# Kernel optimization log

Measured on AMD Instinct MI355X. Metric: run time of the kernel, lower is better.

## Reference

```python
import jax, jax.numpy as jnp
import numpy as np

N = 131072      # 8192 sudoku puzzles x 16 cells
E = 1048576     # random constraint edges (avg degree 8)
HID = 64
NEG_SLOPE = 0.2


def setup_inputs() -> dict:
    key = jax.random.key(0)
    ks = jax.random.split(key, 18)
    p = lambda k, shape: jax.random.normal(k, shape, dtype=jnp.float32) * 0.05
    return {
        "x": jax.random.randint(ks[0], (N,), 0, 5),
        "edge_index": jax.random.randint(ks[1], (2, E), 0, N),
        "emb": p(ks[2], (5, HID)),
        # conv1: in 64 -> heads=4, C=64, concat
        "W1": p(ks[3], (HID, 4 * HID)),
        "a1_src": p(ks[4], (4, HID)),
        "a1_dst": p(ks[5], (4, HID)),
        "b1": p(ks[6], (4 * HID,)),
        # conv2: in 256 -> heads=4, C=64, concat
        "W2": p(ks[7], (4 * HID, 4 * HID)),
        "a2_src": p(ks[8], (4, HID)),
        "a2_dst": p(ks[9], (4, HID)),
        "b2": p(ks[10], (4 * HID,)),
        # conv3: in 256 -> heads=1, C=64, no concat
        "W3": p(ks[11], (4 * HID, HID)),
        "a3_src": p(ks[12], (1, HID)),
        "a3_dst": p(ks[13], (1, HID)),
        "b3": p(ks[14], (HID,)),
        "fc_w": p(ks[15], (HID, 5)),
        "fc_b": p(ks[16], (5,)),
    }


def gat_conv(x, src, dst, W, a_src, a_dst, b, concat):
    """PyG-style GATConv (self-loops already appended to src/dst)."""
    n = x.shape[0]
    H, C = a_src.shape
    h = (x @ W).reshape(n, H, C)                       # [N,H,C]
    alpha_s = jnp.einsum('nhc,hc->nh', h, a_src)       # [N,H]
    alpha_d = jnp.einsum('nhc,hc->nh', h, a_dst)
    e = jax.nn.leaky_relu(alpha_s[src] + alpha_d[dst], NEG_SLOPE)  # [E,H]
    # scatter-softmax over incoming edges per destination node
    e_max = jax.ops.segment_max(e, dst, num_segments=n)
    e_exp = jnp.exp(e - e_max[dst])
    denom = jax.ops.segment_sum(e_exp, dst, num_segments=n)
    alpha = e_exp / (denom[dst] + 1e-16)               # [E,H]
    msg = h[src] * alpha[:, :, None]                   # [E,H,C]
    out = jax.ops.segment_sum(msg, dst, num_segments=n)  # [N,H,C]
    out = out.reshape(n, H * C) if concat else out.mean(axis=1)
    return out + b


def reference(x, edge_index, emb, W1, a1_src, a1_dst, b1,
              W2, a2_src, a2_dst, b2, W3, a3_src, a3_dst, b3, fc_w, fc_b):
    n = x.shape[0]
    loops = jnp.arange(n)
    src = jnp.concatenate([edge_index[0], loops])  # add self-loops (PyG default)
    dst = jnp.concatenate([edge_index[1], loops])
    h = emb[x]                                                    # [N,64]
    h = jax.nn.elu(gat_conv(h, src, dst, W1, a1_src, a1_dst, b1, True))
    h = jax.nn.elu(gat_conv(h, src, dst, W2, a2_src, a2_dst, b2, True))
    h = jax.nn.elu(gat_conv(h, src, dst, W3, a3_src, a3_dst, b3, False))
    return h @ fc_w + fc_b                                        # [N,5]
```

## Files before the change

### kernel.cpp

```cpp
#include <hip/hip_runtime.h>
#include <hip/hip_bf16.h>
#include <hip/hip_fp8.h>

typedef __attribute__((ext_vector_type(8))) short short8;
typedef __attribute__((ext_vector_type(4))) short short4_t;
typedef __attribute__((ext_vector_type(4))) float floatx4;
typedef __attribute__((ext_vector_type(2))) float floatx2;

constexpr int NB  = 256;
constexpr int CAP = 6144;

__device__ __forceinline__ unsigned short f2bf(float f){
  unsigned int u = __float_as_uint(f);
  u += 0x7FFF + ((u >> 16) & 1);
  return (unsigned short)(u >> 16);
}
__device__ __forceinline__ float bf2f(unsigned short h){
  return __uint_as_float(((unsigned int)h) << 16);
}
__device__ __forceinline__ float lrelu(float x){ return x > 0.f ? x : 0.2f * x; }
__device__ __forceinline__ float eluf(float x){ return x > 0.f ? x : (__expf(x) - 1.f); }

__device__ __forceinline__ unsigned char f2fp8(float f){
  __hip_fp8_e4m3 t(f);
  return (unsigned char)t.__x;
}
__device__ __forceinline__ float fp82f(unsigned char b){
  __hip_fp8_e4m3 t;
  t.__x = (__hip_fp8_storage_t)b;
  return (float)t;
}

template<bool HI>
__device__ __forceinline__ floatx2 fp8pk2(unsigned int v){
#if defined(__has_builtin) && __has_builtin(__builtin_amdgcn_cvt_pk_f32_fp8)
  return __builtin_amdgcn_cvt_pk_f32_fp8((int)v, HI);
#else
  floatx2 r;
  constexpr int sh = HI ? 16 : 0;
  r.x = fp82f((unsigned char)((v >> sh) & 0xFF));
  r.y = fp82f((unsigned char)((v >> (sh + 8)) & 0xFF));
  return r;
#endif
}

__device__ __forceinline__ unsigned int f32x4_to_fp8(float a0, float a1, float a2, float a3){
#if defined(__has_builtin) && __has_builtin(__builtin_amdgcn_cvt_pk_fp8_f32)
  int w = 0;
  w = __builtin_amdgcn_cvt_pk_fp8_f32(a0, a1, w, false);
  w = __builtin_amdgcn_cvt_pk_fp8_f32(a2, a3, w, true);
  return (unsigned int)w;
#else
  return (unsigned int)f2fp8(a0) | ((unsigned int)f2fp8(a1) << 8) |
         ((unsigned int)f2fp8(a2) << 16) | ((unsigned int)f2fp8(a3) << 24);
#endif
}

__device__ __forceinline__ void gload16(const unsigned short* g, unsigned short* l){
  __builtin_amdgcn_global_load_lds(
      (const __attribute__((address_space(1))) unsigned int*)(const void*)g,
      (__attribute__((address_space(3))) unsigned int*)(void*)l,
      16, 0, 0);
}


__global__ __launch_bounds__(256) void part_k(const int* __restrict__ ei, int E, int shift,
                                              int* __restrict__ gcnt,
                                              uint2* __restrict__ bbuf){
  __shared__ int hist[NB];
  __shared__ int base[NB];
  int tid = threadIdx.x;
  hist[tid] = 0;
  __syncthreads();
  int blk_start = blockIdx.x * 4096;
  int src[16], bkt[16], lp[16];
  #pragma unroll
  for (int k = 0; k < 16; k++){
    int i = blk_start + k * 256 + tid;
    if (i < E){
      int dst = ei[E + i];
      src[k] = ei[i];
      bkt[k] = dst >> shift;
      lp[k] = atomicAdd(&hist[bkt[k]], 1);
    } else {
      bkt[k] = -1;
    }
  }
  __syncthreads();
  base[tid] = atomicAdd(&gcnt[tid], hist[tid]);
  __syncthreads();
  #pragma unroll
  for (int k = 0; k < 16; k++){
    int i = blk_start + k * 256 + tid;
    if (i < E){
      int b = bkt[k];
      int dst = ei[E + i];
      bbuf[(size_t)b * CAP + base[b] + lp[k]] = make_uint2((unsigned)src[k], (unsigned)dst);
    }
  }
}

__global__ __launch_bounds__(256) void bscan_k(const int* __restrict__ gcnt,
                                               int* __restrict__ gbase,
                                               int* __restrict__ row_ptr, int N, int dpb){
  __shared__ int s[NB];
  int t = threadIdx.x;
  int v = gcnt[t] + dpb;
  s[t] = v;
  __syncthreads();
  #pragma unroll
  for (int off = 1; off < NB; off <<= 1){
    int u = (t >= off) ? s[t - off] : 0;
    __syncthreads();
    s[t] += u;
    __syncthreads();
  }
  gbase[t] = s[t] - v;
  if (t == NB - 1){ gbase[NB] = s[t]; row_ptr[N] = s[t]; }
}

__global__ __launch_bounds__(256) void sort_k(const uint2* __restrict__ bbuf,
                                              const int* __restrict__ gcnt,
                                              const int* __restrict__ gbase,
                                              int* __restrict__ row_ptr,
                                              int* __restrict__ sorted_src, int dpb){
  __shared__ int counts[512];
  __shared__ int curs[512];
  __shared__ int wsum[256];
  __shared__ int sortedL[CAP + 512];
  int b = blockIdx.x, tid = threadIdx.x;
  int cnt = gcnt[b];
  int dstBase = b * dpb;
  int gb = gbase[b];
  counts[tid] = 0;
  counts[tid + 256] = 0;
  __syncthreads();
  for (int i = tid; i < cnt; i += 256){
    uint2 p = bbuf[(size_t)b * CAP + i];
    atomicAdd(&counts[(int)p.y - dstBase], 1);
  }
  __syncthreads();
  int c0 = counts[2 * tid] + 1;
  int c1 = counts[2 * tid + 1] + 1;
  int sum = c0 + c1;
  wsum[tid] = sum;
  __syncthreads();
  #pragma unroll
  for (int off = 1; off < 256; off <<= 1){
    int u = (tid >= off) ? wsum[tid - off] : 0;
    __syncthreads();
    wsum[tid] += u;
    __syncthreads();
  }
  int ex = wsum[tid] - sum;
  int ro0 = ex, ro1 = ex + c0;
  curs[2 * tid] = ro0 + 1;
  curs[2 * tid + 1] = ro1 + 1;
  sortedL[ro0] = dstBase + 2 * tid;
  sortedL[ro1] = dstBase + 2 * tid + 1;
  row_ptr[dstBase + 2 * tid] = gb + ro0;
  row_ptr[dstBase + 2 * tid + 1] = gb + ro1;
  __syncthreads();
  for (int i = tid; i < cnt; i += 256){
    uint2 p = bbuf[(size_t)b * CAP + i];
    int pos = atomicAdd(&curs[(int)p.y - dstBase], 1);
    sortedL[pos] = (int)p.x;
  }
  __syncthreads();
  int tot = cnt + dpb;
  for (int i = tid; i < tot; i += 256) sorted_src[gb + i] = sortedL[i];
}


__global__ __launch_bounds__(256) void prep_k(const float* __restrict__ W2,
                                              unsigned short* __restrict__ Wp2,
                                              const float* __restrict__ W3,
                                              unsigned short* __restrict__ Wp3,
                                              const float* __restrict__ emb,
                                              const float* __restrict__ W1,
                                              const float* __restrict__ a1s,
                                              const float* __restrict__ a1d,
                                              float* __restrict__ T1,
                                              float* __restrict__ wt_tab){
  __shared__ float t_lds[1280];
  __shared__ float as_l[20], ad_l[20];
  int b = blockIdx.x;
  int tid = threadIdx.x;
  if (b < 256){
    int idx = b * 256 + tid;
    int k = idx >> 8, nn = idx & 255;
    Wp2[nn * 256 + k] = f2bf(W2[idx]);
  } else if (b < 320){
    int idx = (b - 256) * 256 + tid;
    int k = idx >> 6, nn = idx & 63;
    Wp3[nn * 256 + k] = f2bf(W3[idx]);
  } else {
    for (int i = tid; i < 1280; i += 256){
      int r = i >> 8, c = i & 255;
      float s = 0.f;
      for (int k = 0; k < 64; k++) s += emb[r * 64 + k] * W1[k * 256 + c];
      t_lds[i] = s;
      T1[i] = s;
    }
    __syncthreads();
    if (tid < 20){
      int r = tid >> 2, hh = tid & 3;
      float ss = 0.f, sd = 0.f;
      for (int c = 0; c < 64; c++){
        float f = t_lds[r * 256 + hh * 64 + c];
        ss += f * a1s[hh * 64 + c];
        sd += f * a1d[hh * 64 + c];
      }
      as_l[tid] = ss;
      ad_l[tid] = sd;
    }
    __syncthreads();
    if (tid < 100){
      int xd = tid / 20, rest = tid % 20;
      int h = rest & 3;
      wt_tab[tid] = __expf(lrelu(as_l[rest] + ad_l[xd * 4 + h]));
    }
  }
}

template<int BN, int MODE, bool F8OUT>
__global__ __launch_bounds__(256) void gemm_lds_k(const unsigned short* __restrict__ A,
                                                  const unsigned short* __restrict__ Wp,
                                                  void* __restrict__ Cout, int Nc,
                                                  const float* __restrict__ a_src,
                                                  const float* __restrict__ a_dst,
                                                  float* __restrict__ as_arr,
                                                  float* __restrict__ ad_arr){
  constexpr int K = 256;
  constexpr int NT = BN / 32;
  __shared__ unsigned short Alds[128 * 32];
  __shared__ unsigned short Blds[BN * 32];
  __shared__ float asl[128], adl[128];
  __shared__ float pas[128][2], pad[128][2];
  int tid = threadIdx.x;
  int w = tid >> 6, l = tid & 63;
  int r16 = l & 15, quad = l >> 4;
  int wr = w >> 1, wc = w & 1;
  int mBase = blockIdx.x * 128;
  int nBase = blockIdx.y * BN;

  if constexpr (MODE == 1){
    if (tid < 128){ asl[tid] = a_src[nBase + tid]; adl[tid] = a_dst[nBase + tid]; }
  }
  if constexpr (MODE == 2){
    if (tid < 64){ asl[tid] = a_src[tid]; adl[tid] = a_dst[tid]; }
  }

  int arow = l >> 2;
  int kcol = (l & 3) * 8;
  const unsigned short* gA0 = A + (size_t)(mBase + w * 32 + arow) * K + kcol;
  const unsigned short* gA1 = gA0 + (size_t)16 * K;
  unsigned short* lA0 = &Alds[(w * 32) * 32];
  unsigned short* lA1 = &Alds[(w * 32 + 16) * 32];
  const unsigned short* gB0;
  const unsigned short* gB1 = nullptr;
  unsigned short* lB0;
  unsigned short* lB1 = nullptr;
  if constexpr (BN == 128){
    gB0 = Wp + (size_t)(nBase + w * 32 + arow) * K + kcol;
    gB1 = gB0 + (size_t)16 * K;
    lB0 = &Blds[(w * 32) * 32];
    lB1 = &Blds[(w * 32 + 16) * 32];
  } else {
    gB0 = Wp + (size_t)(nBase + w * 16 + arow) * K + kcol;
    lB0 = &Blds[(w * 16) * 32];
  }

  floatx4 acc[4][NT];
  #pragma unroll
  for (int mt = 0; mt < 4; mt++)
    #pragma unroll
    for (int nt = 0; nt < NT; nt++){ floatx4 z = {0.f,0.f,0.f,0.f}; acc[mt][nt] = z; }

  for (int kt = 0; kt < 8; kt++){
    int ko = kt * 32;
    gload16(gA0 + ko, lA0);
    gload16(gA1 + ko, lA1);
    gload16(gB0 + ko, lB0);
    if constexpr (BN == 128) gload16(gB1 + ko, lB1);
    __syncthreads();
    short8 af[4], bfr[NT];
    #pragma unroll
    for (int mt = 0; mt < 4; mt++)
      af[mt] = *(const short8*)&Alds[(wr * 64 + mt * 16 + r16) * 32 + quad * 8];
    #pragma unroll
    for (int nt = 0; nt < NT; nt++)
      bfr[nt] = *(const short8*)&Blds[(wc * (BN / 2) + nt * 16 + r16) * 32 + quad * 8];
    #pragma unroll
    for (int mt = 0; mt < 4; mt++)
      #pragma unroll
      for (int nt = 0; nt < NT; nt++)
        acc[mt][nt] = __builtin_amdgcn_mfma_f32_16x16x32_bf16(af[mt], bfr[nt], acc[mt][nt], 0, 0, 0);
    __syncthreads();
  }

  #pragma unroll
  for (int mt = 0; mt < 4; mt++){
    #pragma unroll
    for (int nt = 0; nt < NT; nt++){
      if constexpr (F8OUT){
        unsigned int pk = f32x4_to_fp8(acc[mt][nt][0] * 64.f, acc[mt][nt][1] * 64.f,
                                       acc[mt][nt][2] * 64.f, acc[mt][nt][3] * 64.f);
        int col = nBase + wc * (BN / 2) + nt * 16 + r16;
        int row0 = mBase + wr * 64 + mt * 16 + quad * 4;
        #pragma unroll
        for (int r = 0; r < 4; r++)
          ((unsigned char*)Cout)[(size_t)(row0 + r) * Nc + col] =
              (unsigned char)((pk >> (r * 8)) & 0xFF);
      } else {
        #pragma unroll
        for (int r = 0; r < 4; r++){
          int row = mBase + wr * 64 + mt * 16 + quad * 4 + r;
          int col = nBase + wc * (BN / 2) + nt * 16 + r16;
          ((unsigned short*)Cout)[(size_t)row * Nc + col] = f2bf(acc[mt][nt][r]);
        }
      }
    }
  }
  if constexpr (MODE == 1){
    int head = (nBase + wc * 64) >> 6;
    #pragma unroll
    for (int mt = 0; mt < 4; mt++){
      #pragma unroll
      for (int r = 0; r < 4; r++){
        float ps = 0.f, pd = 0.f;
        #pragma unroll
        for (int nt = 0; nt < NT; nt++){
          float v = acc[mt][nt][r];
          int ci = wc * 64 + nt * 16 + r16;
          ps += v * asl[ci];
          pd += v * adl[ci];
        }
        ps += __shfl_xor(ps, 1, 64); ps += __shfl_xor(ps, 2, 64);
        ps += __shfl_xor(ps, 4, 64); ps += __shfl_xor(ps, 8, 64);
        pd += __shfl_xor(pd, 1, 64); pd += __shfl_xor(pd, 2, 64);
        pd += __shfl_xor(pd, 4, 64); pd += __shfl_xor(pd, 8, 64);
        if (r16 == 0){
          int row = mBase + wr * 64 + mt * 16 + quad * 4 + r;
          as_arr[row * 4 + head] = ps;
          ad_arr[row * 4 + head] = pd;
        }
      }
    }
  }
  if constexpr (MODE == 2){
    #pragma unroll
    for (int mt = 0; mt < 4; mt++){
      #pragma unroll
      for (int r = 0; r < 4; r++){
        float ps = 0.f, pd = 0.f;
        #pragma unroll
        for (int nt = 0; nt < NT; nt++){
          float v = acc[mt][nt][r];
          int ci = wc * 32 + nt * 16 + r16;
          ps += v * asl[ci];
          pd += v * adl[ci];
        }
        ps += __shfl_xor(ps, 1, 64); ps += __shfl_xor(ps, 2, 64);
        ps += __shfl_xor(ps, 4, 64); ps += __shfl_xor(ps, 8, 64);
        pd += __shfl_xor(pd, 1, 64); pd += __shfl_xor(pd, 2, 64);
        pd += __shfl_xor(pd, 4, 64); pd += __shfl_xor(pd, 8, 64);
        if (r16 == 0){
          int lr = wr * 64 + mt * 16 + quad * 4 + r;
          pas[lr][wc] = ps;
          pad[lr][wc] = pd;
        }
      }
    }
    __syncthreads();
    if (tid < 128){
      as_arr[mBase + tid] = pas[tid][0] + pas[tid][1];
      ad_arr[mBase + tid] = pad[tid][0] + pad[tid][1];
    }
  }
}


__global__ __launch_bounds__(256) void agg1_k(const int* __restrict__ x,
                                              const float* __restrict__ T1,
                                              const float* __restrict__ wt_tab,
                                              const int* __restrict__ row_ptr,
                                              const int* __restrict__ sorted_src,
                                              const float* __restrict__ bias,
                                              unsigned short* __restrict__ outb){
  __shared__ float t_lds[1280];
  __shared__ float wt_l[100], b_lds[256];
  __shared__ float cnt_lds[256][5];
  __shared__ int xd_lds[256];
  int tid = threadIdx.x;
  for (int i = tid; i < 1280; i += 256) t_lds[i] = T1[i];
  if (tid < 100) wt_l[tid] = wt_tab[tid];
  b_lds[tid] = bias[tid];
  int d = blockIdx.x * 256 + tid;
  int start = row_ptr[d], end = row_ptr[d + 1];
  xd_lds[tid] = x[d];
  float c0 = 0.f, c1 = 0.f, c2 = 0.f, c3 = 0.f, c4 = 0.f;
  for (int e = start; e < end; e++){
    int xs = x[sorted_src[e]];
    c0 += (xs == 0) ? 1.f : 0.f;
    c1 += (xs == 1) ? 1.f : 0.f;
    c2 += (xs == 2) ? 1.f : 0.f;
    c3 += (xs == 3) ? 1.f : 0.f;
    c4 += (xs == 4) ? 1.f : 0.f;
  }
  cnt_lds[tid][0] = c0; cnt_lds[tid][1] = c1; cnt_lds[tid][2] = c2;
  cnt_lds[tid][3] = c3; cnt_lds[tid][4] = c4;
  __syncthreads();
  int w = tid >> 6, l = tid & 63;
  int head = l >> 4;
  int c0i = l * 4;
  for (int dl = w; dl < 256; dl += 4){
    int dd = blockIdx.x * 256 + dl;
    int xd20 = xd_lds[dl] * 20;
    float ws[5];
    float den = 0.f;
    #pragma unroll
    for (int v2 = 0; v2 < 5; v2++){
      float wv = wt_l[xd20 + v2 * 4 + head] * cnt_lds[dl][v2];
      ws[v2] = wv;
      den += wv;
    }
    float inv = 1.f / (den + 1e-16f);
    float num[4] = {0.f, 0.f, 0.f, 0.f};
    #pragma unroll
    for (int v2 = 0; v2 < 5; v2++){
      const float4 row = *(const float4*)&t_lds[v2 * 256 + c0i];
      num[0] += ws[v2] * row.x;
      num[1] += ws[v2] * row.y;
      num[2] += ws[v2] * row.z;
      num[3] += ws[v2] * row.w;
    }
    short4_t ov;
    #pragma unroll
    for (int j = 0; j < 4; j++)
      ov[j] = (short)f2bf(eluf(num[j] * inv + b_lds[c0i + j]));
    *(short4_t*)(outb + (size_t)dd * 256 + c0i) = ov;
  }
}


__global__ __launch_bounds__(256) void agg4_k(const unsigned char* __restrict__ h8,
                                              const float* __restrict__ as_arr,
                                              const float* __restrict__ ad_arr,
                                              const int* __restrict__ row_ptr,
                                              const int* __restrict__ sorted_src,
                                              const float* __restrict__ bias,
                                              unsigned short* __restrict__ outb){
  __shared__ float b_lds[256];
  int tid = threadIdx.x;
  b_lds[tid] = bias[tid];
  __syncthreads();
  int w = tid >> 6, l = tid & 63;
  int d = blockIdx.x * 4 + w;
  int hl = l & 31, half = l >> 5;
  unsigned head = (unsigned)(hl >> 3);
  unsigned hloff = (unsigned)(hl * 8);
  int start = row_ptr[d], end = row_ptr[d + 1];
  float a_d = ad_arr[d * 4 + head];
  floatx2 ac0 = {0.f, 0.f}, ac1 = {0.f, 0.f}, ac2 = {0.f, 0.f}, ac3 = {0.f, 0.f};
  float den = 0.f;
  int e = start + half;
  for (; e + 6 < end; e += 8){
    unsigned sA = (unsigned)sorted_src[e];
    unsigned sB = (unsigned)sorted_src[e + 2];
    unsigned sC = (unsigned)sorted_src[e + 4];
    unsigned sD = (unsigned)sorted_src[e + 6];
    uint2 vA = *(const uint2*)(h8 + ((sA << 8) | hloff));
    uint2 vB = *(const uint2*)(h8 + ((sB << 8) | hloff));
    uint2 vC = *(const uint2*)(h8 + ((sC << 8) | hloff));
    uint2 vD = *(const uint2*)(h8 + ((sD << 8) | hloff));
    float wgA = __expf(lrelu(as_arr[(sA << 2) + head] + a_d));
    float wgB = __expf(lrelu(as_arr[(sB << 2) + head] + a_d));
    float wgC = __expf(lrelu(as_arr[(sC << 2) + head] + a_d));
    float wgD = __expf(lrelu(as_arr[(sD << 2) + head] + a_d));
    den += (wgA + wgB) + (wgC + wgD);
    floatx2 wA = {wgA, wgA}, wB = {wgB, wgB}, wC = {wgC, wgC}, wD = {wgD, wgD};
    ac0 += wA * fp8pk2<false>(vA.x) + wB * fp8pk2<false>(vB.x)
         + wC * fp8pk2<false>(vC.x) + wD * fp8pk2<false>(vD.x);
    ac1 += wA * fp8pk2<true>(vA.x)  + wB * fp8pk2<true>(vB.x)
         + wC * fp8pk2<true>(vC.x)  + wD * fp8pk2<true>(vD.x);
    ac2 += wA * fp8pk2<false>(vA.y) + wB * fp8pk2<false>(vB.y)
         + wC * fp8pk2<false>(vC.y) + wD * fp8pk2<false>(vD.y);
    ac3 += wA * fp8pk2<true>(vA.y)  + wB * fp8pk2<true>(vB.y)
         + wC * fp8pk2<true>(vC.y)  + wD * fp8pk2<true>(vD.y);
  }
  for (; e + 2 < end; e += 4){
    unsigned sA = (unsigned)sorted_src[e];
    unsigned sB = (unsigned)sorted_src[e + 2];
    uint2 vA = *(const uint2*)(h8 + ((sA << 8) | hloff));
    uint2 vB = *(const uint2*)(h8 + ((sB << 8) | hloff));
    float wgA = __expf(lrelu(as_arr[(sA << 2) + head] + a_d));
    float wgB = __expf(lrelu(as_arr[(sB << 2) + head] + a_d));
    den += wgA + wgB;
    floatx2 wA = {wgA, wgA}, wB = {wgB, wgB};
    ac0 += wA * fp8pk2<false>(vA.x) + wB * fp8pk2<false>(vB.x);
    ac1 += wA * fp8pk2<true>(vA.x)  + wB * fp8pk2<true>(vB.x);
    ac2 += wA * fp8pk2<false>(vA.y) + wB * fp8pk2<false>(vB.y);
    ac3 += wA * fp8pk2<true>(vA.y)  + wB * fp8pk2<true>(vB.y);
  }
  for (; e < end; e += 2){
    unsigned s = (unsigned)sorted_src[e];
    float wg = __expf(lrelu(as_arr[(s << 2) + head] + a_d));
    den += wg;
    uint2 v = *(const uint2*)(h8 + ((s << 8) | hloff));
    floatx2 wv = {wg, wg};
    ac0 += wv * fp8pk2<false>(v.x);
    ac1 += wv * fp8pk2<true>(v.x);
    ac2 += wv * fp8pk2<false>(v.y);
    ac3 += wv * fp8pk2<true>(v.y);
  }
  float acc[8] = {ac0.x, ac0.y, ac1.x, ac1.y, ac2.x, ac2.y, ac3.x, ac3.y};
  #pragma unroll
  for (int j = 0; j < 8; j++) acc[j] += __shfl_xor(acc[j], 32, 64);
  den += __shfl_xor(den, 32, 64);
  if (half == 0){
    float inv = 0.015625f / (den + 1e-16f);
    short8 ov;
    #pragma unroll
    for (int j = 0; j < 8; j++){
      float v = eluf(acc[j] * inv + b_lds[hl * 8 + j]);
      ov[j] = (short)f2bf(v);
    }
    *(short8*)(outb + (size_t)d * 256 + hl * 8) = ov;
  }
}

__global__ __launch_bounds__(256) void agg3_k(const unsigned char* __restrict__ h8,
                                              const float* __restrict__ as_arr,
                                              const float* __restrict__ ad_arr,
                                              const int* __restrict__ row_ptr,
                                              const int* __restrict__ sorted_src,
                                              const float* __restrict__ bias,
                                              unsigned short* __restrict__ outb){
  __shared__ float b_lds[64];
  int tid = threadIdx.x;
  if (tid < 64) b_lds[tid] = bias[tid];
  __syncthreads();
  int w = tid >> 6, l = tid & 63;
  int d = blockIdx.x * 4 + w;
  int q = l & 7, grp = l >> 3;
  unsigned qoff = (unsigned)(q * 8);
  int start = row_ptr[d], end = row_ptr[d + 1];
  float a_d = ad_arr[d];
  floatx2 ac0 = {0.f, 0.f}, ac1 = {0.f, 0.f}, ac2 = {0.f, 0.f}, ac3 = {0.f, 0.f};
  float den = 0.f;
  int e = start + grp;
  for (; e + 8 < end; e += 16){
    unsigned sA = (unsigned)sorted_src[e];
    unsigned sB = (unsigned)sorted_src[e + 8];
    uint2 vA = *(const uint2*)(h8 + ((sA << 6) | qoff));
    uint2 vB = *(const uint2*)(h8 + ((sB << 6) | qoff));
    float wgA = __expf(lrelu(as_arr[sA] + a_d));
    float wgB = __expf(lrelu(as_arr[sB] + a_d));
    den += wgA + wgB;
    floatx2 wA = {wgA, wgA}, wB = {wgB, wgB};
    ac0 += wA * fp8pk2<false>(vA.x) + wB * fp8pk2<false>(vB.x);
    ac1 += wA * fp8pk2<true>(vA.x)  + wB * fp8pk2<true>(vB.x);
    ac2 += wA * fp8pk2<false>(vA.y) + wB * fp8pk2<false>(vB.y);
    ac3 += wA * fp8pk2<true>(vA.y)  + wB * fp8pk2<true>(vB.y);
  }
  for (; e < end; e += 8){
    unsigned s = (unsigned)sorted_src[e];
    float wg = __expf(lrelu(as_arr[s] + a_d));
    den += wg;
    uint2 v = *(const uint2*)(h8 + ((s << 6) | qoff));
    floatx2 wv = {wg, wg};
    ac0 += wv * fp8pk2<false>(v.x);
    ac1 += wv * fp8pk2<true>(v.x);
    ac2 += wv * fp8pk2<false>(v.y);
    ac3 += wv * fp8pk2<true>(v.y);
  }
  float acc[8] = {ac0.x, ac0.y, ac1.x, ac1.y, ac2.x, ac2.y, ac3.x, ac3.y};
  #pragma unroll
  for (int j = 0; j < 8; j++){
    acc[j] += __shfl_xor(acc[j], 8, 64);
    acc[j] += __shfl_xor(acc[j], 16, 64);
    acc[j] += __shfl_xor(acc[j], 32, 64);
  }
  den += __shfl_xor(den, 8, 64);
  den += __shfl_xor(den, 16, 64);
  den += __shfl_xor(den, 32, 64);
  if (l < 8){
    float inv = 0.015625f / (den + 1e-16f);
    short8 ov;
    #pragma unroll
    for (int j = 0; j < 8; j++){
      float v = eluf(acc[j] * inv + b_lds[q * 8 + j]);
      ov[j] = (short)f2bf(v);
    }
    *(short8*)(outb + (size_t)d * 64 + q * 8) = ov;
  }
}


__global__ __launch_bounds__(256) void fc_k(const unsigned short* __restrict__ hb,
                                            const float* __restrict__ fcw,
                                            const float* __restrict__ fcb,
                                            float* __restrict__ out){
  __shared__ float w_lds[320];
  __shared__ float b_lds[5];
  int tid = threadIdx.x;
  for (int i = tid; i < 320; i += 256) w_lds[i] = fcw[i];
  if (tid < 5) b_lds[tid] = fcb[tid];
  __syncthreads();
  int n = blockIdx.x * 256 + tid;
  const short8* p = (const short8*)(hb + (size_t)n * 64);
  float acc[5];
  #pragma unroll
  for (int j = 0; j < 5; j++) acc[j] = b_lds[j];
  #pragma unroll
  for (int b = 0; b < 8; b++){
    short8 v = p[b];
    #pragma unroll
    for (int j8 = 0; j8 < 8; j8++){
      float f = bf2f((unsigned short)v[j8]);
      int k = b * 8 + j8;
      #pragma unroll
      for (int j = 0; j < 5; j++) acc[j] += f * w_lds[k * 5 + j];
    }
  }
  #pragma unroll
  for (int j = 0; j < 5; j++) out[(size_t)n * 5 + j] = acc[j];
}


extern "C" void kernel_launch(void* const* d_in, const int* in_sizes, int n_in,
                              void* d_out, int out_size, void* d_ws, size_t ws_size,
                              hipStream_t stream){
  const int*   x    = (const int*)d_in[0];
  const int*   ei   = (const int*)d_in[1];
  const float* emb  = (const float*)d_in[2];
  const float* W1   = (const float*)d_in[3];
  const float* a1s  = (const float*)d_in[4];
  const float* a1d  = (const float*)d_in[5];
  const float* b1   = (const float*)d_in[6];
  const float* W2   = (const float*)d_in[7];
  const float* a2s  = (const float*)d_in[8];
  const float* a2d  = (const float*)d_in[9];
  const float* b2   = (const float*)d_in[10];
  const float* W3   = (const float*)d_in[11];
  const float* a3s  = (const float*)d_in[12];
  const float* a3d  = (const float*)d_in[13];
  const float* b3   = (const float*)d_in[14];
  const float* fcw  = (const float*)d_in[15];
  const float* fcb  = (const float*)d_in[16];
  float* out = (float*)d_out;

  const int N = in_sizes[0];
  const int E = in_sizes[1] / 2;
  const int dpb = N / NB;
  int shift = 0;
  while ((1 << shift) < dpb) shift++;

  char* base = (char*)d_ws;
  size_t off = 0;
  auto alloc = [&](size_t bytes) -> void* {
    void* p = base + off;
    off += (bytes + 255) & ~(size_t)255;
    return p;
  };
  unsigned short* bufB    = (unsigned short*)alloc((size_t)N * 256 * 2);
  unsigned char*  buf8    = (unsigned char*)alloc((size_t)N * 256);
  float* alpha_s          = (float*)alloc((size_t)N * 4 * 4);
  float* alpha_d          = (float*)alloc((size_t)N * 4 * 4);
  int* row_ptr            = (int*)alloc((size_t)(N + 1) * 4);
  int* sorted_src         = (int*)alloc((size_t)(E + N) * 4);
  uint2* bbuf             = (uint2*)alloc((size_t)NB * CAP * 8);
  int* gcnt               = (int*)alloc((size_t)NB * 4);
  int* gbase              = (int*)alloc((size_t)(NB + 1) * 4);
  float* T1               = (float*)alloc(5 * 256 * 4);
  float* wt_tab           = (float*)alloc(100 * 4);
  unsigned short* Wp2     = (unsigned short*)alloc(256 * 256 * 2);
  unsigned short* Wp3     = (unsigned short*)alloc(64 * 256 * 2);

  (void)hipMemsetAsync(gcnt, 0, (size_t)NB * 4, stream);
  part_k<<<(E + 4095) / 4096, 256, 0, stream>>>(ei, E, shift, gcnt, bbuf);
  bscan_k<<<1, 256, 0, stream>>>(gcnt, gbase, row_ptr, N, dpb);
  sort_k<<<NB, 256, 0, stream>>>(bbuf, gcnt, gbase, row_ptr, sorted_src, dpb);

  prep_k<<<321, 256, 0, stream>>>(W2, Wp2, W3, Wp3, emb, W1, a1s, a1d, T1, wt_tab);

  agg1_k<<<N / 256, 256, 0, stream>>>(x, T1, wt_tab, row_ptr, sorted_src, b1, bufB);

  gemm_lds_k<128, 1, true><<<dim3(N / 128, 2), 256, 0, stream>>>(bufB, Wp2, buf8, 256,
                                                                 a2s, a2d, alpha_s, alpha_d);
  agg4_k<<<N / 4, 256, 0, stream>>>(buf8, alpha_s, alpha_d, row_ptr, sorted_src, b2, bufB);

  gemm_lds_k<64, 2, true><<<dim3(N / 128, 1), 256, 0, stream>>>(bufB, Wp3, buf8, 64,
                                                                a3s, a3d, alpha_s, alpha_d);
  agg3_k<<<N / 4, 256, 0, stream>>>(buf8, alpha_s, alpha_d, row_ptr, sorted_src, b3, bufB);

  fc_k<<<N / 256, 256, 0, stream>>>(bufB, fcw, fcb, out);
}
```

Baseline: 360.7 us.

## Precompute per-edge attention weights for layer 2 and swizzle GEMM block order

Adds a sorted_dst array emitted by the sort kernel and a new ew4_k kernel that computes exp(leaky_relu(alpha_s[src]+alpha_d[dst])) for all four heads per edge into a dense buffer. The layer-2 aggregation then reads these weights sequentially instead of gathering alpha_s and evaluating exp per head inside its loop. The middle 2-edge unrolled tail is dropped. The layer-2 GEMM now uses a 1D grid with a swizzle that groups the two N-tiles of the same row blocks together for A reuse. In exchange the sort kernel's LDS use roughly doubles and about 20 MB of extra edge-weight traffic plus one launch is added.

```diff
diff --git a/kernel.cpp b/kernel.cpp
--- a/kernel.cpp
+++ b/kernel.cpp
@@ -123,11 +123,13 @@
                                               const int* __restrict__ gcnt,
                                               const int* __restrict__ gbase,
                                               int* __restrict__ row_ptr,
-                                              int* __restrict__ sorted_src, int dpb){
+                                              int* __restrict__ sorted_src,
+                                              int* __restrict__ sorted_dst, int dpb){
   __shared__ int counts[512];
   __shared__ int curs[512];
   __shared__ int wsum[256];
   __shared__ int sortedL[CAP + 512];
+  __shared__ int dstL[CAP + 512];
   int b = blockIdx.x, tid = threadIdx.x;
   int cnt = gcnt[b];
   int dstBase = b * dpb;
@@ -158,6 +160,8 @@
   curs[2 * tid + 1] = ro1 + 1;
   sortedL[ro0] = dstBase + 2 * tid;
   sortedL[ro1] = dstBase + 2 * tid + 1;
+  dstL[ro0] = dstBase + 2 * tid;
+  dstL[ro1] = dstBase + 2 * tid + 1;
   row_ptr[dstBase + 2 * tid] = gb + ro0;
   row_ptr[dstBase + 2 * tid + 1] = gb + ro1;
   __syncthreads();
@@ -165,10 +169,32 @@
     uint2 p = bbuf[(size_t)b * CAP + i];
     int pos = atomicAdd(&curs[(int)p.y - dstBase], 1);
     sortedL[pos] = (int)p.x;
+    dstL[pos] = (int)p.y;
   }
   __syncthreads();
   int tot = cnt + dpb;
-  for (int i = tid; i < tot; i += 256) sorted_src[gb + i] = sortedL[i];
+  for (int i = tid; i < tot; i += 256){
+    sorted_src[gb + i] = sortedL[i];
+    sorted_dst[gb + i] = dstL[i];
+  }
+}
+
+__global__ __launch_bounds__(256) void ew4_k(const int* __restrict__ ss,
+                                             const int* __restrict__ sd,
+                                             const float4* __restrict__ as4,
+                                             const float4* __restrict__ ad4,
+                                             float4* __restrict__ ew, int tot){
+  int e = blockIdx.x * 256 + threadIdx.x;
+  if (e < tot){
+    float4 a = as4[ss[e]];
+    float4 b = ad4[sd[e]];
+    float4 o;
+    o.x = __expf(lrelu(a.x + b.x));
+    o.y = __expf(lrelu(a.y + b.y));
+    o.z = __expf(lrelu(a.z + b.z));
+    o.w = __expf(lrelu(a.w + b.w));
+    ew[e] = o;
+  }
 }
 
 
@@ -223,7 +249,7 @@
   }
 }
 
-template<int BN, int MODE, bool F8OUT>
+template<int BN, int MODE, bool F8OUT, bool SWZ>
 __global__ __launch_bounds__(256) void gemm_lds_k(const unsigned short* __restrict__ A,
                                                   const unsigned short* __restrict__ Wp,
                                                   void* __restrict__ Cout, int Nc,
@@ -241,8 +267,18 @@
   int w = tid >> 6, l = tid & 63;
   int r16 = l & 15, quad = l >> 4;
   int wr = w >> 1, wc = w & 1;
-  int mBase = blockIdx.x * 128;
-  int nBase = blockIdx.y * BN;
+  int bx, by;
+  if constexpr (SWZ){
+    int b = blockIdx.x;
+    int g = b >> 4, i = b & 15;
+    bx = g * 8 + (i & 7);
+    by = i >> 3;
+  } else {
+    bx = blockIdx.x;
+    by = blockIdx.y;
+  }
+  int mBase = bx * 128;
+  int nBase = by * BN;
 
   if constexpr (MODE == 1){
     if (tid < 128){ asl[tid] = a_src[nBase + tid]; adl[tid] = a_dst[nBase + tid]; }
@@ -445,8 +481,7 @@
 
 
 __global__ __launch_bounds__(256) void agg4_k(const unsigned char* __restrict__ h8,
-                                              const float* __restrict__ as_arr,
-                                              const float* __restrict__ ad_arr,
+                                              const float* __restrict__ ewf,
                                               const int* __restrict__ row_ptr,
                                               const int* __restrict__ sorted_src,
                                               const float* __restrict__ bias,
@@ -461,7 +496,6 @@
   unsigned head = (unsigned)(hl >> 3);
   unsigned hloff = (unsigned)(hl * 8);
   int start = row_ptr[d], end = row_ptr[d + 1];
-  float a_d = ad_arr[d * 4 + head];
   floatx2 ac0 = {0.f, 0.f}, ac1 = {0.f, 0.f}, ac2 = {0.f, 0.f}, ac3 = {0.f, 0.f};
   float den = 0.f;
   int e = start + half;
@@ -474,10 +508,10 @@
     uint2 vB = *(const uint2*)(h8 + ((sB << 8) | hloff));
     uint2 vC = *(const uint2*)(h8 + ((sC << 8) | hloff));
     uint2 vD = *(const uint2*)(h8 + ((sD << 8) | hloff));
-    float wgA = __expf(lrelu(as_arr[(sA << 2) + head] + a_d));
-    float wgB = __expf(lrelu(as_arr[(sB << 2) + head] + a_d));
-    float wgC = __expf(lrelu(as_arr[(sC << 2) + head] + a_d));
-    float wgD = __expf(lrelu(as_arr[(sD << 2) + head] + a_d));
+    float wgA = ewf[((unsigned)e << 2) + head];
+    float wgB = ewf[(((unsigned)e + 2) << 2) + head];
+    float wgC = ewf[(((unsigned)e + 4) << 2) + head];
+    float wgD = ewf[(((unsigned)e + 6) << 2) + head];
     den += (wgA + wgB) + (wgC + wgD);
     floatx2 wA = {wgA, wgA}, wB = {wgB, wgB}, wC = {wgC, wgC}, wD = {wgD, wgD};
     ac0 += wA * fp8pk2<false>(vA.x) + wB * fp8pk2<false>(vB.x)
@@ -489,23 +523,9 @@
     ac3 += wA * fp8pk2<true>(vA.y)  + wB * fp8pk2<true>(vB.y)
          + wC * fp8pk2<true>(vC.y)  + wD * fp8pk2<true>(vD.y);
   }
-  for (; e + 2 < end; e += 4){
-    unsigned sA = (unsigned)sorted_src[e];
-    unsigned sB = (unsigned)sorted_src[e + 2];
-    uint2 vA = *(const uint2*)(h8 + ((sA << 8) | hloff));
-    uint2 vB = *(const uint2*)(h8 + ((sB << 8) | hloff));
-    float wgA = __expf(lrelu(as_arr[(sA << 2) + head] + a_d));
-    float wgB = __expf(lrelu(as_arr[(sB << 2) + head] + a_d));
-    den += wgA + wgB;
-    floatx2 wA = {wgA, wgA}, wB = {wgB, wgB};
-    ac0 += wA * fp8pk2<false>(vA.x) + wB * fp8pk2<false>(vB.x);
-    ac1 += wA * fp8pk2<true>(vA.x)  + wB * fp8pk2<true>(vB.x);
-    ac2 += wA * fp8pk2<false>(vA.y) + wB * fp8pk2<false>(vB.y);
-    ac3 += wA * fp8pk2<true>(vA.y)  + wB * fp8pk2<true>(vB.y);
-  }
   for (; e < end; e += 2){
     unsigned s = (unsigned)sorted_src[e];
-    float wg = __expf(lrelu(as_arr[(s << 2) + head] + a_d));
+    float wg = ewf[((unsigned)e << 2) + head];
     den += wg;
     uint2 v = *(const uint2*)(h8 + ((s << 8) | hloff));
     floatx2 wv = {wg, wg};
@@ -529,6 +549,7 @@
     *(short8*)(outb + (size_t)d * 256 + hl * 8) = ov;
   }
 }
+
 
 __global__ __launch_bounds__(256) void agg3_k(const unsigned char* __restrict__ h8,
                                               const float* __restrict__ as_arr,
@@ -653,6 +674,7 @@
 
   const int N = in_sizes[0];
   const int E = in_sizes[1] / 2;
+  const int Etot = E + N;
   const int dpb = N / NB;
   int shift = 0;
   while ((1 << shift) < dpb) shift++;
@@ -669,7 +691,9 @@
   float* alpha_s          = (float*)alloc((size_t)N * 4 * 4);
   float* alpha_d          = (float*)alloc((size_t)N * 4 * 4);
   int* row_ptr            = (int*)alloc((size_t)(N + 1) * 4);
-  int* sorted_src         = (int*)alloc((size_t)(E + N) * 4);
+  int* sorted_src         = (int*)alloc((size_t)Etot * 4);
+  int* sorted_dst         = (int*)alloc((size_t)Etot * 4);
+  float* ew               = (float*)alloc((size_t)Etot * 4 * 4);
   uint2* bbuf             = (uint2*)alloc((size_t)NB * CAP * 8);
   int* gcnt               = (int*)alloc((size_t)NB * 4);
   int* gbase              = (int*)alloc((size_t)(NB + 1) * 4);
@@ -681,18 +705,21 @@
   (void)hipMemsetAsync(gcnt, 0, (size_t)NB * 4, stream);
   part_k<<<(E + 4095) / 4096, 256, 0, stream>>>(ei, E, shift, gcnt, bbuf);
   bscan_k<<<1, 256, 0, stream>>>(gcnt, gbase, row_ptr, N, dpb);
-  sort_k<<<NB, 256, 0, stream>>>(bbuf, gcnt, gbase, row_ptr, sorted_src, dpb);
+  sort_k<<<NB, 256, 0, stream>>>(bbuf, gcnt, gbase, row_ptr, sorted_src, sorted_dst, dpb);
 
   prep_k<<<321, 256, 0, stream>>>(W2, Wp2, W3, Wp3, emb, W1, a1s, a1d, T1, wt_tab);
 
   agg1_k<<<N / 256, 256, 0, stream>>>(x, T1, wt_tab, row_ptr, sorted_src, b1, bufB);
 
-  gemm_lds_k<128, 1, true><<<dim3(N / 128, 2), 256, 0, stream>>>(bufB, Wp2, buf8, 256,
-                                                                 a2s, a2d, alpha_s, alpha_d);
-  agg4_k<<<N / 4, 256, 0, stream>>>(buf8, alpha_s, alpha_d, row_ptr, sorted_src, b2, bufB);
-
-  gemm_lds_k<64, 2, true><<<dim3(N / 128, 1), 256, 0, stream>>>(bufB, Wp3, buf8, 64,
-                                                                a3s, a3d, alpha_s, alpha_d);
+  gemm_lds_k<128, 1, true, true><<<(N / 128) * 2, 256, 0, stream>>>(bufB, Wp2, buf8, 256,
+                                                                    a2s, a2d, alpha_s, alpha_d);
+  ew4_k<<<(Etot + 255) / 256, 256, 0, stream>>>(sorted_src, sorted_dst,
+                                                (const float4*)alpha_s, (const float4*)alpha_d,
+                                                (float4*)ew, Etot);
+  agg4_k<<<N / 4, 256, 0, stream>>>(buf8, ew, row_ptr, sorted_src, b2, bufB);
+
+  gemm_lds_k<64, 2, true, false><<<dim3(N / 128, 1), 256, 0, stream>>>(bufB, Wp3, buf8, 64,
+                                                                       a3s, a3d, alpha_s, alpha_d);
   agg3_k<<<N / 4, 256, 0, stream>>>(buf8, alpha_s, alpha_d, row_ptr, sorted_src, b3, bufB);
 
   fc_k<<<N / 256, 256, 0, stream>>>(bufB, fcw, fcb, out);
```

Measured after the change: 369.4 us. 2.4% more time.
